# Kernel tuning notes

Hardware: AMD Instinct MI355X
Metric: run time of the kernel (lower is better)

## Reference

```python
import jax, jax.numpy as jnp
import numpy as np

KEY_CH = 256

def _conv1x1(w, b, t):
    # 1x1 conv with BN folded: t [B,Cin,N] -> [B,Cout,N]
    return jnp.einsum('oc,bcn->bon', w, t) + b[None, :, None]

def _conv1x1_relu(w, b, t):
    return jax.nn.relu(_conv1x1(w, b, t))

def setup_inputs() -> dict:
    key = jax.random.key(0)
    ks = jax.random.split(key, 12)
    B, C, H, W = 4, 512, 128, 128
    d = {}
    d['feat'] = jax.random.normal(ks[0], (B, C, H, W), jnp.float32)
    d['prob'] = jax.random.normal(ks[1], (B, 20, H, W), jnp.float32)  # unused by forward (overwritten)
    s = 0.02
    d['wp1'] = jax.random.normal(ks[2], (KEY_CH, C), jnp.float32) * s
    d['bp1'] = jnp.zeros((KEY_CH,), jnp.float32)
    d['wp2'] = jax.random.normal(ks[3], (KEY_CH, KEY_CH), jnp.float32) * s
    d['bp2'] = jnp.zeros((KEY_CH,), jnp.float32)
    d['wo1'] = jax.random.normal(ks[4], (KEY_CH, C), jnp.float32) * s
    d['bo1'] = jnp.zeros((KEY_CH,), jnp.float32)
    d['wo2'] = jax.random.normal(ks[5], (KEY_CH, KEY_CH), jnp.float32) * s
    d['bo2'] = jnp.zeros((KEY_CH,), jnp.float32)
    d['wd'] = jax.random.normal(ks[6], (KEY_CH, C), jnp.float32) * s
    d['bd'] = jnp.zeros((KEY_CH,), jnp.float32)
    d['wu'] = jax.random.normal(ks[7], (C, KEY_CH), jnp.float32) * s
    d['bu'] = jnp.zeros((C,), jnp.float32)
    d['wout'] = jax.random.normal(ks[8], (512, 2 * C), jnp.float32) * s
    d['bout'] = jnp.zeros((512,), jnp.float32)
    return d


def reference(feat, prob, wp1, bp1, wp2, bp2, wo1, bo1, wo2, bo2, wd, bd, wu, bu, wout, bout):
    B, C, H, W = feat.shape
    x = feat.reshape(B, C, H * W)  # [B,C,N]
    # prob = upsample_bilinear(feat, (H,W)) == feat (identity resize); prob arg is dead.
    # SpatialGather (scale=1): softmax over spatial, weighted pool of features.
    pw = jax.nn.softmax(x, axis=-1)                     # [B,K,N], K == C here
    context = jnp.einsum('bkn,bcn->bck', pw, x)         # [B,C,K] proxy features
    # ObjectAttentionBlock2D
    q = _conv1x1_relu(wp2, bp2, _conv1x1_relu(wp1, bp1, x))        # [B,key,N]
    k = _conv1x1_relu(wo2, bo2, _conv1x1_relu(wo1, bo1, context))  # [B,key,K]
    v = _conv1x1_relu(wd, bd, context)                             # [B,key,K]
    sim = jnp.einsum('bdn,bdk->bnk', q, k) * (KEY_CH ** -0.5)      # [B,N,K]
    sim = jax.nn.softmax(sim, axis=-1)
    ctx = jnp.einsum('bnk,bdk->bdn', sim, v)                       # [B,key,N]
    ctx = _conv1x1_relu(wu, bu, ctx)                               # [B,C,N]
    # SpatialOCR: concat + 1x1 conv + BN + ReLU (dropout identity at eval)
    out = _conv1x1_relu(wout, bout, jnp.concatenate([ctx, x], axis=1))  # [B,out,N]
    return out.reshape(B, -1, H, W)
```

## Files before the change

### kernel.cpp

```cpp
#include <hip/hip_runtime.h>

typedef unsigned int u32;
typedef unsigned short u16;
typedef short s16x8 __attribute__((ext_vector_type(8)));
typedef float f32x4 __attribute__((ext_vector_type(4)));

__device__ __forceinline__ u16 f2bf(float f) {
  u32 u = __float_as_uint(f);
  u32 r = (u + 0x7fffu + ((u >> 16) & 1u)) >> 16;
  return (u16)r;
}

template <int MODE>
__device__ __forceinline__ uint4 pack8(const float* p, float2 st) {
  float4 f0 = *(const float4*)p;
  float4 f1 = *(const float4*)(p + 4);
  float v[8] = {f0.x, f0.y, f0.z, f0.w, f1.x, f1.y, f1.z, f1.w};
  if (MODE == 2) {
#pragma unroll
    for (int j = 0; j < 8; ++j) v[j] = __expf(v[j] - st.x) * st.y;
  }
  uint4 o;
  o.x = (u32)f2bf(v[0]) | ((u32)f2bf(v[1]) << 16);
  o.y = (u32)f2bf(v[2]) | ((u32)f2bf(v[3]) << 16);
  o.z = (u32)f2bf(v[4]) | ((u32)f2bf(v[5]) << 16);
  o.w = (u32)f2bf(v[6]) | ((u32)f2bf(v[7]) << 16);
  return o;
}

__device__ __forceinline__ void g2l16(u16* lds, const u16* g) {
  __builtin_amdgcn_global_load_lds(
      (const __attribute__((address_space(1))) void*)g,
      (__attribute__((address_space(3))) void*)lds, 16, 0, 0);
}

__global__ __launch_bounds__(256) void row_softmax_bf16(
    const float* __restrict__ feat, u16* __restrict__ expx,
    u16* __restrict__ xbf) {
  const long long row = blockIdx.x;
  const float* xp = feat + row * 16384;
  const int tid = threadIdx.x, wv = tid >> 6, ln = tid & 63;
  __shared__ float red[4];
  float4 v[16];
  float mx = -1e30f;
#pragma unroll
  for (int p = 0; p < 16; ++p) {
    v[p] = *(const float4*)(xp + tid * 4 + p * 1024);
    mx = fmaxf(mx, fmaxf(fmaxf(v[p].x, v[p].y), fmaxf(v[p].z, v[p].w)));
  }
  u16* bp = xbf + row * 16384;
#pragma unroll
  for (int p = 0; p < 16; ++p) {
    uint2 ow;
    ow.x = (u32)f2bf(v[p].x) | ((u32)f2bf(v[p].y) << 16);
    ow.y = (u32)f2bf(v[p].z) | ((u32)f2bf(v[p].w) << 16);
    *(uint2*)(bp + tid * 4 + p * 1024) = ow;
  }
  for (int o = 32; o; o >>= 1) mx = fmaxf(mx, __shfl_xor(mx, o, 64));
  if (!ln) red[wv] = mx;
  __syncthreads();
  mx = fmaxf(fmaxf(red[0], red[1]), fmaxf(red[2], red[3]));
  __syncthreads();
  float s = 0.f;
#pragma unroll
  for (int p = 0; p < 16; ++p) {
    v[p].x = __expf(v[p].x - mx);
    v[p].y = __expf(v[p].y - mx);
    v[p].z = __expf(v[p].z - mx);
    v[p].w = __expf(v[p].w - mx);
    s += v[p].x + v[p].y + v[p].z + v[p].w;
  }
  for (int o = 32; o; o >>= 1) s += __shfl_xor(s, o, 64);
  if (!ln) red[wv] = s;
  __syncthreads();
  const float inv = 1.f / (red[0] + red[1] + red[2] + red[3]);
  u16* op = expx + row * 16384;
#pragma unroll
  for (int p = 0; p < 16; ++p) {
    uint2 ow;
    ow.x = (u32)f2bf(v[p].x * inv) | ((u32)f2bf(v[p].y * inv) << 16);
    ow.y = (u32)f2bf(v[p].z * inv) | ((u32)f2bf(v[p].w * inv) << 16);
    *(uint2*)(op + tid * 4 + p * 1024) = ow;
  }
}

__global__ __launch_bounds__(256) void transpose_x(const u16* __restrict__ xbf,
                                                   u16* __restrict__ catT) {
  __shared__ u16 t[32][33];
  const int b = blockIdx.z;
  const int c0 = blockIdx.y << 5, n0 = blockIdx.x << 5;
  const int tx = threadIdx.x & 31, ty = threadIdx.x >> 5;
  const u16* fb = xbf + (long long)b * 512 * 16384;
#pragma unroll
  for (int i = 0; i < 32; i += 8)
    t[ty + i][tx] = fb[(long long)(c0 + ty + i) * 16384 + n0 + tx];
  __syncthreads();
  u16* ob = catT + (long long)b * 16384 * 1024 + 512;
#pragma unroll
  for (int i = 0; i < 32; i += 8)
    ob[(long long)(n0 + ty + i) * 1024 + c0 + tx] = t[tx][ty + i];
}

__global__ __launch_bounds__(256) void cvt_weights(
    const float* __restrict__ w0, const float* __restrict__ w1,
    const float* __restrict__ w2, const float* __restrict__ w3,
    const float* __restrict__ w4, const float* __restrict__ w5,
    const float* __restrict__ w6, u16* __restrict__ dst) {
  const long long i = (long long)blockIdx.x * 256 + threadIdx.x;
  const float* s;
  long long off;
  if (i < 131072) { s = w0; off = 0; }
  else if (i < 196608) { s = w1; off = 131072; }
  else if (i < 327680) { s = w2; off = 196608; }
  else if (i < 393216) { s = w3; off = 327680; }
  else if (i < 524288) { s = w4; off = 393216; }
  else if (i < 655360) { s = w5; off = 524288; }
  else { s = w6; off = 655360; }
  dst[i] = f2bf(s[i - off]);
}

template <int ACT, int BIAS, int SPLITK, int AMODE, int BMODE, int F32OUT>
__global__ __launch_bounds__(256, 2) void gemm_nt(
    const void* __restrict__ Av, long long sA, int lda,
    const void* __restrict__ Bv, long long sB, int ldb,
    void* __restrict__ C, long long sC, int ldc,
    const float* __restrict__ bias, int K, int kchunk,
    const float2* __restrict__ stats, int statsStride) {
  __shared__ __align__(16) u16 Asm_[128 * 32];
  __shared__ __align__(16) u16 Bsm_[128 * 32];
  const int tid = threadIdx.x;
  const int wv = tid >> 6;
  const int ln = tid & 63;
  const int bz = blockIdx.z;
  const int batch = SPLITK ? (bz >> 3) : bz;
  const int chunk = SPLITK ? (bz & 7) : 0;
  const long long tm = (long long)blockIdx.y << 7;
  const long long tn = (long long)blockIdx.x << 7;
  const int lrow = ln >> 2;
  const int lcol = (ln & 3) << 3;
  const int w32 = wv << 5;
  const long long ar0 = tm + w32 + lrow, ar1 = ar0 + 16;
  const long long br0 = tn + w32 + lrow, br1 = br0 + 16;
  const long long koff = (long long)chunk * kchunk + lcol;
  const u16* gau0; const u16* gau1; const float* gaf0; const float* gaf1;
  if (AMODE == 0) {
    const u16* Ab = (const u16*)Av + (long long)batch * sA + koff;
    gau0 = Ab + ar0 * lda; gau1 = Ab + ar1 * lda; gaf0 = gaf1 = nullptr;
  } else {
    const float* Ab = (const float*)Av + (long long)batch * sA + koff;
    gaf0 = Ab + ar0 * lda; gaf1 = Ab + ar1 * lda; gau0 = gau1 = nullptr;
  }
  const u16* gbu0; const u16* gbu1; const float* gbf0; const float* gbf1;
  if (BMODE == 0) {
    const u16* Bb = (const u16*)Bv + (long long)batch * sB + koff;
    gbu0 = Bb + br0 * ldb; gbu1 = Bb + br1 * ldb; gbf0 = gbf1 = nullptr;
  } else {
    const float* Bb = (const float*)Bv + (long long)batch * sB + koff;
    gbf0 = Bb + br0 * ldb; gbf1 = Bb + br1 * ldb; gbu0 = gbu1 = nullptr;
  }
  float2 stA0 = make_float2(0.f, 0.f), stA1 = stA0;
  if (AMODE == 2) {
    stA0 = stats[batch * statsStride + (int)ar0];
    stA1 = stats[batch * statsStride + (int)ar1];
  }
  u16* la0 = &Asm_[w32 * 32];
  u16* la1 = la0 + 512;
  u16* lb0 = &Bsm_[w32 * 32];
  u16* lb1 = lb0 + 512;
  const int fr = ln & 15;
  const int fq = ln >> 4;
  const int wm = (wv >> 1) << 6;
  const int wn = (wv & 1) << 6;
  f32x4 acc[4][4] = {};
  for (int kk = 0; kk < K; kk += 32) {
    if (AMODE == 0 && BMODE == 0) {
      __syncthreads();
      g2l16(la0, gau0 + kk);
      g2l16(la1, gau1 + kk);
      g2l16(lb0, gbu0 + kk);
      g2l16(lb1, gbu1 + kk);
      __syncthreads();
    } else {
      uint4 ra0, ra1, rb0, rb1;
      if (AMODE == 0) {
        ra0 = *(const uint4*)(gau0 + kk);
        ra1 = *(const uint4*)(gau1 + kk);
      } else {
        ra0 = pack8<AMODE>(gaf0 + kk, stA0);
        ra1 = pack8<AMODE>(gaf1 + kk, stA1);
      }
      if (BMODE == 0) {
        rb0 = *(const uint4*)(gbu0 + kk);
        rb1 = *(const uint4*)(gbu1 + kk);
      } else {
        rb0 = pack8<BMODE>(gbf0 + kk, stA0);
        rb1 = pack8<BMODE>(gbf1 + kk, stA1);
      }
      __syncthreads();
      *(uint4*)(la0 + ln * 8) = ra0;
      *(uint4*)(la1 + ln * 8) = ra1;
      *(uint4*)(lb0 + ln * 8) = rb0;
      *(uint4*)(lb1 + ln * 8) = rb1;
      __syncthreads();
    }
    s16x8 af[4], bfr[4];
#pragma unroll
    for (int i = 0; i < 4; ++i)
      af[i] = *(const s16x8*)&Asm_[(wm + i * 16 + fr) * 32 + fq * 8];
#pragma unroll
    for (int j = 0; j < 4; ++j)
      bfr[j] = *(const s16x8*)&Bsm_[(wn + j * 16 + fr) * 32 + fq * 8];
#pragma unroll
    for (int i = 0; i < 4; ++i)
#pragma unroll
      for (int j = 0; j < 4; ++j)
        acc[i][j] =
            __builtin_amdgcn_mfma_f32_16x16x32_bf16(af[i], bfr[j], acc[i][j], 0, 0, 0);
  }
#pragma unroll
  for (int i = 0; i < 4; ++i) {
    const long long gr0 = tm + wm + i * 16 + fq * 4;
#pragma unroll
    for (int j = 0; j < 4; ++j) {
      const long long gc = tn + wn + j * 16 + fr;
      float bc = 0.f;
      if (BIAS == 2) bc = bias[gc];
#pragma unroll
      for (int t = 0; t < 4; ++t) {
        float v = acc[i][j][t];
        if (BIAS == 1) v += bias[gr0 + t];
        if (BIAS == 2) v += bc;
        if (ACT) v = fmaxf(v, 0.f);
        const long long idx = (long long)batch * sC + (gr0 + t) * ldc + gc;
        if (SPLITK)
          atomicAdd((float*)C + idx, v);
        else if (F32OUT)
          ((float*)C)[idx] = v;
        else
          ((u16*)C)[idx] = f2bf(v);
      }
    }
  }
}

__global__ __launch_bounds__(256) void cvt_f32_bf16(const float* __restrict__ s,
                                                    u16* __restrict__ d) {
  const int i = blockIdx.x * 256 + threadIdx.x;
  d[i] = f2bf(s[i]);
}

__global__ __launch_bounds__(256) void softmax_p(u16* __restrict__ P) {
  const int wv = threadIdx.x >> 6, ln = threadIdx.x & 63;
  const long long row = (long long)blockIdx.x * 4 + wv;
  u16* rp = P + row * 1024;
  uint4 r = *(const uint4*)(rp + ln * 8);
  u32 w[4] = {r.x, r.y, r.z, r.w};
  float v[8];
#pragma unroll
  for (int k = 0; k < 4; ++k) {
    v[2 * k] = __uint_as_float(w[k] << 16) * 0.0625f;
    v[2 * k + 1] = __uint_as_float(w[k] & 0xffff0000u) * 0.0625f;
  }
  float m = v[0];
#pragma unroll
  for (int t = 1; t < 8; ++t) m = fmaxf(m, v[t]);
  for (int o = 32; o; o >>= 1) m = fmaxf(m, __shfl_xor(m, o, 64));
  float e[8], s = 0.f;
#pragma unroll
  for (int t = 0; t < 8; ++t) {
    e[t] = __expf(v[t] - m);
    s += e[t];
  }
  for (int o = 32; o; o >>= 1) s += __shfl_xor(s, o, 64);
  const float inv = 1.f / s;
  u32 ow[4];
#pragma unroll
  for (int k = 0; k < 4; ++k)
    ow[k] = (u32)f2bf(e[2 * k] * inv) | ((u32)f2bf(e[2 * k + 1] * inv) << 16);
  *(uint4*)(rp + ln * 8) = make_uint4(ow[0], ow[1], ow[2], ow[3]);
}

extern "C" void kernel_launch(void* const* d_in, const int* in_sizes, int n_in,
                              void* d_out, int out_size, void* d_ws, size_t ws_size,
                              hipStream_t stream) {
  const float* feat = (const float*)d_in[0];
  const float* wp1 = (const float*)d_in[2];
  const float* bp1 = (const float*)d_in[3];
  const float* wp2 = (const float*)d_in[4];
  const float* bp2 = (const float*)d_in[5];
  const float* wo1 = (const float*)d_in[6];
  const float* bo1 = (const float*)d_in[7];
  const float* wo2 = (const float*)d_in[8];
  const float* bo2 = (const float*)d_in[9];
  const float* wd = (const float*)d_in[10];
  const float* bd = (const float*)d_in[11];
  const float* wu = (const float*)d_in[12];
  const float* bu = (const float*)d_in[13];
  const float* wout = (const float*)d_in[14];
  const float* bout = (const float*)d_in[15];
  float* outp = (float*)d_out;
  char* ws = (char*)d_ws;

  u16* catT = (u16*)ws;
  u16* expx = (u16*)(ws + 134217728LL);
  u16* q1T = (u16*)(ws + 134217728LL);
  u16* ctxT = q1T;
  u16* qT = (u16*)(ws + 167772160LL);
  float* ctxF = (float*)(ws + 201326592LL);
  u16* wb = (u16*)(ws + 201326592LL);
  u16* conT = (u16*)(ws + 205520896LL);
  u16* k1hT = (u16*)(ws + 207618048LL);
  u16* kTm = (u16*)(ws + 208666624LL);
  u16* vm = (u16*)(ws + 209715200LL);
  if (ws_size < 210763776ULL) return;
  u16* xbf = (u16*)d_out;
  u16* wp1b = wb + 0;
  u16* wp2b = wb + 131072;
  u16* wo1b = wb + 196608;
  u16* wo2b = wb + 327680;
  u16* wdb = wb + 393216;
  u16* wub = wb + 524288;
  u16* woutb = wb + 655360;

  row_softmax_bf16<<<2048, 256, 0, stream>>>(feat, expx, xbf);
  transpose_x<<<dim3(512, 16, 4), 256, 0, stream>>>(xbf, catT);
  hipMemsetAsync(ctxF, 0, 4194304, stream);
  gemm_nt<0, 0, 1, 0, 0, 0><<<dim3(4, 4, 32), 256, 0, stream>>>(
      expx, 8388608LL, 16384, xbf, 8388608LL, 16384, ctxF, 262144LL, 512,
      nullptr, 2048, 2048, nullptr, 0);
  cvt_f32_bf16<<<4096, 256, 0, stream>>>(ctxF, conT);
  cvt_weights<<<4608, 256, 0, stream>>>(wp1, wp2, wo1, wo2, wd, wu, wout, wb);
  gemm_nt<1, 2, 0, 0, 0, 0><<<dim3(2, 4, 4), 256, 0, stream>>>(
      conT, 262144LL, 512, wo1b, 0LL, 512, k1hT, 131072LL, 256, bo1, 512, 0,
      nullptr, 0);
  gemm_nt<1, 2, 0, 0, 0, 0><<<dim3(2, 4, 4), 256, 0, stream>>>(
      k1hT, 131072LL, 256, wo2b, 0LL, 256, kTm, 131072LL, 256, bo2, 256, 0,
      nullptr, 0);
  gemm_nt<1, 1, 0, 0, 0, 0><<<dim3(4, 2, 4), 256, 0, stream>>>(
      wdb, 0LL, 512, conT, 262144LL, 512, vm, 131072LL, 512, bd, 512, 0,
      nullptr, 0);
  gemm_nt<1, 2, 0, 0, 0, 0><<<dim3(2, 128, 4), 256, 0, stream>>>(
      catT + 512, 16777216LL, 1024, wp1b, 0LL, 512, q1T, 4194304LL, 256, bp1,
      512, 0, nullptr, 0);
  gemm_nt<1, 2, 0, 0, 0, 0><<<dim3(2, 128, 4), 256, 0, stream>>>(
      q1T, 4194304LL, 256, wp2b, 0LL, 256, qT, 4194304LL, 256, bp2, 256, 0,
      nullptr, 0);
  gemm_nt<0, 0, 0, 0, 0, 0><<<dim3(4, 128, 4), 256, 0, stream>>>(
      qT, 4194304LL, 256, kTm, 131072LL, 256, catT, 16777216LL, 1024, nullptr,
      256, 0, nullptr, 0);
  softmax_p<<<16384, 256, 0, stream>>>(catT);
  gemm_nt<0, 0, 0, 0, 0, 0><<<dim3(2, 128, 4), 256, 0, stream>>>(
      catT, 16777216LL, 1024, vm, 131072LL, 512, ctxT, 4194304LL, 256, nullptr,
      512, 0, nullptr, 0);
  gemm_nt<1, 2, 0, 0, 0, 0><<<dim3(4, 128, 4), 256, 0, stream>>>(
      ctxT, 4194304LL, 256, wub, 0LL, 256, catT, 16777216LL, 1024, bu, 256, 0,
      nullptr, 0);
  gemm_nt<1, 1, 0, 0, 0, 1><<<dim3(128, 4, 4), 256, 0, stream>>>(
      woutb, 0LL, 1024, catT, 16777216LL, 1024, outp, 8388608LL, 16384, bout,
      1024, 0, nullptr, 0);
}
```

Measured before the change: 674.4 us.

## Double-buffer LDS in bf16 GEMM with XOR swizzle and higher occupancy

The bf16 path of the GEMM kernel now double-buffers its LDS tiles. The next K-slice is staged with direct global-to-LDS loads while the MFMAs run on the current slice, replacing the two barriers per iteration with a single wait-and-barrier. An XOR swizzle on the K-column offset is applied on both the store and load sides to cut LDS bank conflicts on fragment reads. Launch bounds rise to 4 blocks per CU, which doubles LDS per block and may raise register pressure or cause spills.

```diff
diff --git a/kernel.cpp b/kernel.cpp
--- a/kernel.cpp
+++ b/kernel.cpp
@@ -120,14 +120,14 @@
 }
 
 template <int ACT, int BIAS, int SPLITK, int AMODE, int BMODE, int F32OUT>
-__global__ __launch_bounds__(256, 2) void gemm_nt(
+__global__ __launch_bounds__(256, 4) void gemm_nt(
     const void* __restrict__ Av, long long sA, int lda,
     const void* __restrict__ Bv, long long sB, int ldb,
     void* __restrict__ C, long long sC, int ldc,
     const float* __restrict__ bias, int K, int kchunk,
     const float2* __restrict__ stats, int statsStride) {
-  __shared__ __align__(16) u16 Asm_[128 * 32];
-  __shared__ __align__(16) u16 Bsm_[128 * 32];
+  __shared__ __align__(16) u16 Asm_[2][128 * 32];
+  __shared__ __align__(16) u16 Bsm_[2][128 * 32];
   const int tid = threadIdx.x;
   const int wv = tid >> 6;
   const int ln = tid & 63;
@@ -137,7 +137,7 @@
   const long long tm = (long long)blockIdx.y << 7;
   const long long tn = (long long)blockIdx.x << 7;
   const int lrow = ln >> 2;
-  const int lcol = (ln & 3) << 3;
+  const int lcol = (((ln & 3) ^ ((ln >> 3) & 3)) << 3);
   const int w32 = wv << 5;
   const long long ar0 = tm + w32 + lrow, ar1 = ar0 + 16;
   const long long br0 = tn + w32 + lrow, br1 = br0 + 16;
@@ -163,24 +163,45 @@
     stA0 = stats[batch * statsStride + (int)ar0];
     stA1 = stats[batch * statsStride + (int)ar1];
   }
-  u16* la0 = &Asm_[w32 * 32];
-  u16* la1 = la0 + 512;
-  u16* lb0 = &Bsm_[w32 * 32];
-  u16* lb1 = lb0 + 512;
   const int fr = ln & 15;
   const int fq = ln >> 4;
   const int wm = (wv >> 1) << 6;
   const int wn = (wv & 1) << 6;
+  const int rx = (fq ^ ((fr >> 1) & 3)) << 3;
   f32x4 acc[4][4] = {};
-  for (int kk = 0; kk < K; kk += 32) {
-    if (AMODE == 0 && BMODE == 0) {
-      __syncthreads();
-      g2l16(la0, gau0 + kk);
-      g2l16(la1, gau1 + kk);
-      g2l16(lb0, gbu0 + kk);
-      g2l16(lb1, gbu1 + kk);
-      __syncthreads();
-    } else {
+  if (AMODE == 0 && BMODE == 0) {
+    auto stage = [&](int bo, int kk) {
+      g2l16(&Asm_[0][bo + w32 * 32], gau0 + kk);
+      g2l16(&Asm_[0][bo + w32 * 32 + 512], gau1 + kk);
+      g2l16(&Bsm_[0][bo + w32 * 32], gbu0 + kk);
+      g2l16(&Bsm_[0][bo + w32 * 32 + 512], gbu1 + kk);
+    };
+    stage(0, 0);
+    asm volatile("s_waitcnt vmcnt(0)" ::: "memory");
+    asm volatile("s_barrier" ::: "memory");
+    int cb = 0;
+    for (int kk = 0; kk < K; kk += 32) {
+      s16x8 af[4], bfr[4];
+#pragma unroll
+      for (int i = 0; i < 4; ++i)
+        af[i] = *(const s16x8*)&Asm_[0][cb + (wm + i * 16 + fr) * 32 + rx];
+#pragma unroll
+      for (int j = 0; j < 4; ++j)
+        bfr[j] = *(const s16x8*)&Bsm_[0][cb + (wn + j * 16 + fr) * 32 + rx];
+      if (kk + 32 < K) stage(cb ^ 4096, kk + 32);
+#pragma unroll
+      for (int i = 0; i < 4; ++i)
+#pragma unroll
+        for (int j = 0; j < 4; ++j)
+          acc[i][j] = __builtin_amdgcn_mfma_f32_16x16x32_bf16(
+              af[i], bfr[j], acc[i][j], 0, 0, 0);
+      __builtin_amdgcn_sched_barrier(0);
+      asm volatile("s_waitcnt vmcnt(0) lgkmcnt(0)" ::: "memory");
+      asm volatile("s_barrier" ::: "memory");
+      cb ^= 4096;
+    }
+  } else {
+    for (int kk = 0; kk < K; kk += 32) {
       uint4 ra0, ra1, rb0, rb1;
       if (AMODE == 0) {
         ra0 = *(const uint4*)(gau0 + kk);
@@ -197,25 +218,25 @@
         rb1 = pack8<BMODE>(gbf1 + kk, stA1);
       }
       __syncthreads();
-      *(uint4*)(la0 + ln * 8) = ra0;
-      *(uint4*)(la1 + ln * 8) = ra1;
-      *(uint4*)(lb0 + ln * 8) = rb0;
-      *(uint4*)(lb1 + ln * 8) = rb1;
+      *(uint4*)&Asm_[0][w32 * 32 + ln * 8] = ra0;
+      *(uint4*)&Asm_[0][w32 * 32 + 512 + ln * 8] = ra1;
+      *(uint4*)&Bsm_[0][w32 * 32 + ln * 8] = rb0;
+      *(uint4*)&Bsm_[0][w32 * 32 + 512 + ln * 8] = rb1;
       __syncthreads();
+      s16x8 af[4], bfr[4];
+#pragma unroll
+      for (int i = 0; i < 4; ++i)
+        af[i] = *(const s16x8*)&Asm_[0][(wm + i * 16 + fr) * 32 + rx];
+#pragma unroll
+      for (int j = 0; j < 4; ++j)
+        bfr[j] = *(const s16x8*)&Bsm_[0][(wn + j * 16 + fr) * 32 + rx];
+#pragma unroll
+      for (int i = 0; i < 4; ++i)
+#pragma unroll
+        for (int j = 0; j < 4; ++j)
+          acc[i][j] = __builtin_amdgcn_mfma_f32_16x16x32_bf16(
+              af[i], bfr[j], acc[i][j], 0, 0, 0);
     }
-    s16x8 af[4], bfr[4];
-#pragma unroll
-    for (int i = 0; i < 4; ++i)
-      af[i] = *(const s16x8*)&Asm_[(wm + i * 16 + fr) * 32 + fq * 8];
-#pragma unroll
-    for (int j = 0; j < 4; ++j)
-      bfr[j] = *(const s16x8*)&Bsm_[(wn + j * 16 + fr) * 32 + fq * 8];
-#pragma unroll
-    for (int i = 0; i < 4; ++i)
-#pragma unroll
-      for (int j = 0; j < 4; ++j)
-        acc[i][j] =
-            __builtin_amdgcn_mfma_f32_16x16x32_bf16(af[i], bfr[j], acc[i][j], 0, 0, 0);
   }
 #pragma unroll
   for (int i = 0; i < 4; ++i) {
```

After: 676.6 us. Within noise of the previous version (+0.3%).
